# Optimization experiments

Hardware: AMD Instinct MI355X
Metric: run time of the kernel (lower is better)

The kernel has to match this reference:

```python
import jax, jax.numpy as jnp
import numpy as np

V, D, L, H, FF, B, S = 32000, 2048, 4, 16, 8192, 2, 2048
DH = D // H
PRUNE_LAYERS = (1, 2)   # layers with an attached pruning module
KEEP_RATIO = 0.5        # keep_ratio arg of forward_prefill_with_pruning


def _rms(x, w, eps=1e-6):
    return x * w * jax.lax.rsqrt(jnp.mean(x * x, -1, keepdims=True) + eps)


def _rope(x):
    # x: [B,H,s,DH]; position_ids = arange(s), recomputed after every pruning step
    s = x.shape[2]
    half = DH // 2
    inv = 1.0 / (10000.0 ** (jnp.arange(half, dtype=jnp.float32) / half))
    ang = jnp.arange(s, dtype=jnp.float32)[:, None] * inv  # [s, half]
    cos, sin = jnp.cos(ang), jnp.sin(ang)
    x1, x2 = x[..., :half], x[..., half:]
    return jnp.concatenate([x1 * cos - x2 * sin, x1 * sin + x2 * cos], -1)


def _block(h, mask, wq, wk, wv, wo, wg, wu, wd, ln1, ln2):
    b, s, _ = h.shape
    hn = _rms(h, ln1)
    q = _rope((hn @ wq).reshape(b, s, H, DH).transpose(0, 2, 1, 3))
    k = _rope((hn @ wk).reshape(b, s, H, DH).transpose(0, 2, 1, 3))
    v = (hn @ wv).reshape(b, s, H, DH).transpose(0, 2, 1, 3)
    att = jnp.einsum('bhqd,bhkd->bhqk', q, k) / np.float32(np.sqrt(DH))
    allowed = jnp.tril(jnp.ones((s, s), bool)) & (mask[:, None, None, :] > 0)
    att = jnp.where(allowed, att, jnp.float32(-1e9))
    o = jnp.einsum('bhqk,bhkd->bhqd', jax.nn.softmax(att, -1), v)
    h = h + o.transpose(0, 2, 1, 3).reshape(b, s, D) @ wo
    hn = _rms(h, ln2)
    h = h + (jax.nn.silu(hn @ wg) * (hn @ wu)) @ wd
    return h


def _forward(input_ids, attention_mask, embed, wq, wk, wv, wo, wg, wu, wd, ln1, ln2, lnf, lm_head, scorer):
    h = embed[input_ids]        # [B,S,D]
    mask = attention_mask
    for i in range(L):
        if i in PRUNE_LAYERS:
            pi = PRUNE_LAYERS.index(i)
            # pruning module: Linear(D->2); keep score = logits[..., 0]
            sc = jnp.einsum('bsd,cd->bsc', h, scorer[pi])[..., 0]
            kk = max(1, int(h.shape[1] * KEEP_RATIO))      # static under jit
            _, idx = jax.lax.top_k(sc, kk)
            idx = jnp.sort(idx, -1)                        # sorted kept indices
            h = jnp.take_along_axis(h, idx[..., None], axis=1)
            mask = jnp.take_along_axis(mask, idx, axis=1)
        h = _block(h, mask, wq[i], wk[i], wv[i], wo[i], wg[i], wu[i], wd[i], ln1[i], ln2[i])
    return _rms(h, lnf) @ lm_head   # logits [B, S_pruned, V]


def setup_inputs() -> dict:
    key = jax.random.key(0)
    ks = jax.random.split(key, 12)
    g = lambda k, shape: jax.random.normal(k, shape, jnp.float32) * 0.02
    return {
        'input_ids': jax.random.randint(ks[0], (B, S), 0, V, jnp.int32),
        'attention_mask': jnp.ones((B, S), jnp.int32),
        'embed': g(ks[1], (V, D)),
        'wq': g(ks[2], (L, D, D)),
        'wk': g(ks[3], (L, D, D)),
        'wv': g(ks[4], (L, D, D)),
        'wo': g(ks[5], (L, D, D)),
        'wg': g(ks[6], (L, D, FF)),
        'wu': g(ks[7], (L, D, FF)),
        'wd': g(ks[8], (L, FF, D)),
        'ln1': jnp.ones((L, D), jnp.float32),
        'ln2': jnp.ones((L, D), jnp.float32),
        'lnf': jnp.ones((D,), jnp.float32),
        'lm_head': g(ks[9], (D, V)),
        'scorer': g(ks[10], (len(PRUNE_LAYERS), 2, D)),
    }


def reference(input_ids, attention_mask, embed, wq, wk, wv, wo, wg, wu, wd, ln1, ln2, lnf, lm_head, scorer):
    return _forward(input_ids, attention_mask, embed, wq, wk, wv, wo, wg, wu, wd, ln1, ln2, lnf, lm_head, scorer)
```

## Files before the change

### kernel.cpp

```cpp
#include <hip/hip_runtime.h>
#include <math.h>


#define DD 2048
#define HH 16
#define DHH 128
#define FFF 8192
#define BBATCH 2
#define SSEQ 2048
#define VV 32000
#define LLAYERS 4

typedef float4 f4;
typedef __attribute__((ext_vector_type(8))) short short8;
typedef __attribute__((ext_vector_type(4))) float f32x4;
typedef unsigned short u16;

__device__ inline u16 bf16rne(float x) {
    unsigned u = __float_as_uint(x);
    unsigned r = (u + 0x7FFFu + ((u >> 16) & 1u)) >> 16;
    return (u16)r;
}
__device__ inline float bf16tof(u16 h) {
    return __uint_as_float(((unsigned)h) << 16);
}

__device__ __forceinline__ void gload16(const u16* g, u16* l) {
    __builtin_amdgcn_global_load_lds(
        (const __attribute__((address_space(1))) unsigned int*)g,
        (__attribute__((address_space(3))) unsigned int*)l, 16, 0, 0);
}

#define BARRIER() do { asm volatile("" ::: "memory"); \
    __builtin_amdgcn_s_barrier(); asm volatile("" ::: "memory"); } while (0)

__device__ __forceinline__ void xcd_swz(int& bx, int& by) {
    int gy = gridDim.y;
    int nwg = gridDim.x * gy;
    int orig = bx * gy + by;
    int q = nwg >> 3, r = nwg & 7;
    int xcd = orig & 7, loc = orig >> 3;
    int swz = (xcd < r ? xcd * (q + 1) : r * (q + 1) + (xcd - r) * q) + loc;
    bx = swz / gy;
    by = swz % gy;
}

__global__ void k_embed(const int* __restrict__ ids, const float* __restrict__ emb,
                        float* __restrict__ out) {
    int row = blockIdx.x;
    int id  = ids[row];
    const f4* src = (const f4*)(emb + (size_t)id * DD);
    f4*       dst = (f4*)(out + (size_t)row * DD);
    for (int i = threadIdx.x; i < DD / 4; i += blockDim.x) dst[i] = src[i];
}

__global__ void k_copy_int(const int* __restrict__ src, int* __restrict__ dst, int n) {
    int i = blockIdx.x * blockDim.x + threadIdx.x;
    if (i < n) dst[i] = src[i];
}

__global__ void k_addN(float* __restrict__ H, const float* __restrict__ P,
                       long len, int nparts) {
    long i = (long)blockIdx.x * 256 + threadIdx.x;
    if (i >= len / 4) return;
    f4 h = ((f4*)H)[i];
    for (int z = 0; z < nparts; z++) {
        f4 p = ((const f4*)(P + (size_t)z * len))[i];
        h.x += p.x; h.y += p.y; h.z += p.z; h.w += p.w;
    }
    ((f4*)H)[i] = h;
}

__global__ __launch_bounds__(256) void k_rmsnorm_cvt(const float* __restrict__ x,
                                                     const float* __restrict__ w,
                                                     u16* __restrict__ OH,
                                                     u16* __restrict__ OL) {
    int row = blockIdx.x;
    const float* xr = x + (size_t)row * DD;
    float ss = 0.f;
    for (int i = threadIdx.x; i < DD / 4; i += blockDim.x) {
        f4 v = ((const f4*)xr)[i];
        ss += v.x * v.x + v.y * v.y + v.z * v.z + v.w * v.w;
    }
    for (int o = 32; o > 0; o >>= 1) ss += __shfl_down(ss, o);
    __shared__ float red[4];
    int wid = threadIdx.x >> 6, lane = threadIdx.x & 63;
    if (lane == 0) red[wid] = ss;
    __syncthreads();
    float tot = red[0] + red[1] + red[2] + red[3];
    float inv = 1.0f / sqrtf(tot / (float)DD + 1e-6f);
    for (int i = threadIdx.x; i < DD / 4; i += blockDim.x) {
        f4 v = ((const f4*)xr)[i];
        f4 wv = ((const f4*)w)[i];
        float o[4];
        o[0] = v.x * wv.x * inv; o[1] = v.y * wv.y * inv;
        o[2] = v.z * wv.z * inv; o[3] = v.w * wv.w * inv;
        ushort4 hv, lv;
        u16* hp = (u16*)&hv; u16* lp = (u16*)&lv;
#pragma unroll
        for (int j = 0; j < 4; j++) {
            u16 h = bf16rne(o[j]);
            hp[j] = h;
            lp[j] = bf16rne(o[j] - bf16tof(h));
        }
        *(ushort4*)&OH[(size_t)row * DD + i * 4] = hv;
        *(ushort4*)&OL[(size_t)row * DD + i * 4] = lv;
    }
}

__global__ __launch_bounds__(256) void k_cvt_w(const float* __restrict__ W,
                                               u16* __restrict__ WtH,
                                               u16* __restrict__ WtL,
                                               int K, int N, int nc0, int dn0,
                                               int writeLo) {
    __shared__ float T[64][65];
    int tid = threadIdx.x;
    int n0g = nc0 + blockIdx.x * 64;
    int k0  = blockIdx.y * 64;
#pragma unroll
    for (int it = 0; it < 4; it++) {
        int r = it * 16 + (tid >> 4);
        int c4 = (tid & 15) * 4;
        f4 v = *(const f4*)(W + (size_t)(k0 + r) * N + n0g + c4);
        T[r][c4 + 0] = v.x; T[r][c4 + 1] = v.y;
        T[r][c4 + 2] = v.z; T[r][c4 + 3] = v.w;
    }
    __syncthreads();
    int nl = tid >> 2;
    int ks = (tid & 3) * 16;
    u16 hi[16], lo[16];
#pragma unroll
    for (int j = 0; j < 16; j++) {
        float v = T[ks + j][nl];
        u16 h = bf16rne(v);
        hi[j] = h;
        lo[j] = bf16rne(v - bf16tof(h));
    }
    size_t base = (size_t)(dn0 + blockIdx.x * 64 + nl) * K + k0 + ks;
    *(short8*)&WtH[base]     = *(short8*)&hi[0];
    *(short8*)&WtH[base + 8] = *(short8*)&hi[8];
    if (writeLo) {
        *(short8*)&WtL[base]     = *(short8*)&lo[0];
        *(short8*)&WtL[base + 8] = *(short8*)&lo[8];
    }
}

template <int PASSES, int RES, int DUAL>
__global__ __launch_bounds__(256, 2) void k_bgemm(const u16* __restrict__ AH,
                                                  const u16* __restrict__ AL,
                                                  const u16* __restrict__ B1H,
                                                  const u16* __restrict__ B1L,
                                                  const u16* __restrict__ B2H,
                                                  const u16* __restrict__ B2L,
                                                  const float* __restrict__ Rsrc,
                                                  float* __restrict__ C,
                                                  u16* __restrict__ OH,
                                                  u16* __restrict__ OL,
                                                  int M, int ldC, int K) {
    constexpr int NW = DUAL ? 2 : 1;
    __shared__ u16 As[128 * 32];
    __shared__ u16 Bs[NW][128 * 32];
    int tid = threadIdx.x;
    int bx = blockIdx.x, by = blockIdx.y;
    xcd_swz(bx, by);
    int m0 = by * 128, n0 = bx * 128;
    int lane = tid & 63, w = tid >> 6;
    int wm = w >> 1, wn = w & 1;
    int lr = lane & 15, lq = lane >> 4;
    int grow = lane >> 2;
    int gcol = (lane & 3) * 8;

    f32x4 acc[NW][4][4];
#pragma unroll
    for (int u = 0; u < NW; u++)
#pragma unroll
        for (int i = 0; i < 4; i++)
#pragma unroll
            for (int j = 0; j < 4; j++)
#pragma unroll
                for (int r = 0; r < 4; r++) acc[u][i][j][r] = 0.f;

    const int KT = PASSES * K;
    for (int kb = 0; kb < KT; kb += 32) {
        int p  = (PASSES > 1) ? ((kb >= 2 * K) ? 2 : ((kb >= K) ? 1 : 0)) : 0;
        int ks = kb - p * K;
        const u16* Ab = ((p == 2) ? AL  : AH)  + (size_t)(m0 + w * 32) * K + ks;
        const u16* Bb = ((p == 1) ? B1L : B1H) + (size_t)(n0 + w * 32) * K + ks;
        __syncthreads();
        gload16(Ab + (size_t)grow * K + gcol,        &As[w * 1024]);
        gload16(Ab + (size_t)(grow + 16) * K + gcol, &As[w * 1024 + 512]);
        gload16(Bb + (size_t)grow * K + gcol,        &Bs[0][w * 1024]);
        gload16(Bb + (size_t)(grow + 16) * K + gcol, &Bs[0][w * 1024 + 512]);
        if constexpr (DUAL) {
            const u16* B2b = ((p == 1) ? B2L : B2H) + (size_t)(n0 + w * 32) * K + ks;
            gload16(B2b + (size_t)grow * K + gcol,        &Bs[1][w * 1024]);
            gload16(B2b + (size_t)(grow + 16) * K + gcol, &Bs[1][w * 1024 + 512]);
        }
        __syncthreads();
        short8 a[4];
#pragma unroll
        for (int i = 0; i < 4; i++)
            a[i] = *(const short8*)&As[(wm * 64 + i * 16 + lr) * 32 + lq * 8];
#pragma unroll
        for (int u = 0; u < NW; u++) {
#pragma unroll
            for (int j = 0; j < 4; j++) {
                short8 b = *(const short8*)&Bs[u][(wn * 64 + j * 16 + lr) * 32 + lq * 8];
#pragma unroll
                for (int i = 0; i < 4; i++)
                    acc[u][i][j] = __builtin_amdgcn_mfma_f32_16x16x32_bf16(
                        a[i], b, acc[u][i][j], 0, 0, 0);
            }
        }
    }
#pragma unroll
    for (int i = 0; i < 4; i++) {
#pragma unroll
        for (int j = 0; j < 4; j++) {
            int gm = m0 + wm * 64 + i * 16 + lq * 4;
            int gn = n0 + wn * 64 + j * 16 + lr;
#pragma unroll
            for (int r = 0; r < 4; r++) {
                size_t off = (size_t)(gm + r) * ldC + gn;
                if constexpr (DUAL) {
                    float g = acc[0][i][j][r], uu = acc[1][i][j][r];
                    float v = g / (1.0f + expf(-g)) * uu;
                    u16 h = bf16rne(v);
                    OH[off] = h;
                    OL[off] = bf16rne(v - bf16tof(h));
                } else {
                    float v = acc[0][i][j][r];
                    if constexpr (RES) v += Rsrc[off];
                    C[off] = v;
                }
            }
        }
    }
}

template <int PASSES, int PLANE, int EPI>
__global__ __launch_bounds__(512, 2) void k_bg256(const u16* __restrict__ AH,
                                                  const u16* __restrict__ AL,
                                                  const u16* __restrict__ BH,
                                                  const u16* __restrict__ BL,
                                                  float* __restrict__ C,
                                                  u16* __restrict__ OH,
                                                  u16* __restrict__ OL,
                                                  const u16* __restrict__ GEH,
                                                  const u16* __restrict__ GEL,
                                                  int M, int ldC, int K, int ld) {
    __shared__ u16 SM[65536];
    int tid = threadIdx.x;
    int bx = blockIdx.x, by = blockIdx.y;
    xcd_swz(bx, by);
    {
        size_t zo = (size_t)blockIdx.z * K;
        AH += zo; BH += zo;
        if constexpr (PASSES > 1) { AL += zo; BL += zo; }
        if constexpr (!PLANE) C += (size_t)blockIdx.z * ((size_t)M * ldC);
    }
    int m0 = by * 256, n0 = bx * 256;
    int w = tid >> 6, lane = tid & 63;
    int wm = w >> 2, wn = w & 3;
    int lr = lane & 15, lq = lane >> 4;

    f32x4 acc[8][4];
#pragma unroll
    for (int i = 0; i < 8; i++)
#pragma unroll
        for (int j = 0; j < 4; j++)
#pragma unroll
            for (int r = 0; r < 4; r++) acc[i][j][r] = 0.f;

    auto ASRC = [&](int T) -> const u16* {
        int kb = T * 64;
        if (PASSES > 1) {
            if (kb >= 2 * K) return AL + (kb - 2 * K);
            if (kb >= K)     return AH + (kb - K);
        }
        return AH + kb;
    };
    auto BSRC = [&](int T) -> const u16* {
        int kb = T * 64;
        if (PASSES > 1) {
            if (kb >= 2 * K) return BH + (kb - 2 * K);
            if (kb >= K)     return BL + (kb - K);
        }
        return BH + kb;
    };
    int srr = lane >> 3;
    int scc = ((lane & 7) ^ srr) * 8;
    auto STAGE_A = [&](int T, int h, int buf) {
        const u16* s = ASRC(T) + (size_t)(m0 + h * 128 + w * 16 + srr) * ld + scc;
        u16* d = SM + buf * 32768 + h * 8192 + w * 16 * 64;
        gload16(s, d);
        gload16(s + (size_t)8 * ld, d + 8 * 64);
    };
    auto STAGE_B = [&](int T, int h, int buf) {
        const u16* s = BSRC(T) + (size_t)(n0 + h * 128 + w * 16 + srr) * ld + scc;
        u16* d = SM + buf * 32768 + 16384 + h * 8192 + w * 16 * 64;
        gload16(s, d);
        gload16(s + (size_t)8 * ld, d + 8 * 64);
    };
    auto RD_A = [&](const u16* SMb, int MH, short8 (&aF)[4][2]) {
        const u16* Ab = SMb + MH * 8192;
#pragma unroll
        for (int i = 0; i < 4; i++)
#pragma unroll
            for (int kk = 0; kk < 2; kk++)
                aF[i][kk] = *(const short8*)&Ab[(wm * 64 + i * 16 + lr) * 64 +
                                                (((kk * 4 + lq) ^ (lr & 7)) * 8)];
    };
    auto RD_B = [&](const u16* SMb, int NH, short8 (&bF)[2][2]) {
        const u16* Bb = SMb + 16384 + NH * 8192;
#pragma unroll
        for (int j = 0; j < 2; j++)
#pragma unroll
            for (int kk = 0; kk < 2; kk++)
                bF[j][kk] = *(const short8*)&Bb[(wn * 32 + j * 16 + lr) * 64 +
                                                (((kk * 4 + lq) ^ (lr & 7)) * 8)];
    };

    const int NT = (PASSES * K) >> 6;
    STAGE_A(0, 0, 0); STAGE_B(0, 0, 0);
    STAGE_A(0, 1, 0); STAGE_B(0, 1, 0);
    asm volatile("s_waitcnt vmcnt(0)" ::: "memory");
    BARRIER();

    for (int T = 0; T < NT; T++) {
        int cur = T & 1;
        const u16* SMb = SM + cur * 32768;
        short8 a0[4][2], a1[4][2], b0[2][2], b1[2][2];
        if (T + 1 < NT) { STAGE_A(T + 1, 0, cur ^ 1); STAGE_B(T + 1, 0, cur ^ 1); }
        RD_A(SMb, 0, a0);
        RD_B(SMb, 0, b0);
        if (T + 1 < NT) { STAGE_A(T + 1, 1, cur ^ 1); STAGE_B(T + 1, 1, cur ^ 1); }
        RD_B(SMb, 1, b1);
        RD_A(SMb, 1, a1);
        __builtin_amdgcn_s_setprio(1);
#pragma unroll
        for (int kk = 0; kk < 2; kk++)
#pragma unroll
            for (int j = 0; j < 2; j++)
#pragma unroll
                for (int i = 0; i < 4; i++)
                    acc[i][j] = __builtin_amdgcn_mfma_f32_16x16x32_bf16(
                        a0[i][kk], b0[j][kk], acc[i][j], 0, 0, 0);
#pragma unroll
        for (int kk = 0; kk < 2; kk++)
#pragma unroll
            for (int j = 0; j < 2; j++)
#pragma unroll
                for (int i = 0; i < 4; i++)
                    acc[i][2 + j] = __builtin_amdgcn_mfma_f32_16x16x32_bf16(
                        a0[i][kk], b1[j][kk], acc[i][2 + j], 0, 0, 0);
#pragma unroll
        for (int kk = 0; kk < 2; kk++)
#pragma unroll
            for (int j = 0; j < 2; j++)
#pragma unroll
                for (int i = 0; i < 4; i++)
                    acc[4 + i][j] = __builtin_amdgcn_mfma_f32_16x16x32_bf16(
                        a1[i][kk], b0[j][kk], acc[4 + i][j], 0, 0, 0);
#pragma unroll
        for (int kk = 0; kk < 2; kk++)
#pragma unroll
            for (int j = 0; j < 2; j++)
#pragma unroll
                for (int i = 0; i < 4; i++)
                    acc[4 + i][2 + j] = __builtin_amdgcn_mfma_f32_16x16x32_bf16(
                        a1[i][kk], b1[j][kk], acc[4 + i][2 + j], 0, 0, 0);
        __builtin_amdgcn_s_setprio(0);
        if (T + 1 < NT) {
            asm volatile("s_waitcnt vmcnt(0)" ::: "memory");
            BARRIER();
        }
    }

#pragma unroll
    for (int i16 = 0; i16 < 8; i16++) {
#pragma unroll
        for (int jj = 0; jj < 4; jj++) {
            int gm = m0 + (i16 >> 2) * 128 + wm * 64 + (i16 & 3) * 16 + lq * 4;
            int gn = n0 + (jj >> 1) * 128 + wn * 32 + (jj & 1) * 16 + lr;
#pragma unroll
            for (int r = 0; r < 4; r++) {
                size_t off = (size_t)(gm + r) * ldC + gn;
                float v = acc[i16][jj][r];
                if constexpr (PLANE) {
                    if constexpr (EPI) {
                        float g = bf16tof(GEH[off]) + bf16tof(GEL[off]);
                        v = g / (1.0f + expf(-g)) * v;
                    }
                    u16 h = bf16rne(v);
                    OH[off] = h;
                    OL[off] = bf16rne(v - bf16tof(h));
                } else {
                    C[off] = v;
                }
            }
        }
    }
}

__global__ void k_rope_table(float* __restrict__ cosT, float* __restrict__ sinT) {
    int idx = blockIdx.x * blockDim.x + threadIdx.x;
    if (idx >= SSEQ * 64) return;
    int pos = idx >> 6, d = idx & 63;
    float p   = (float)pow(10000.0, (double)d * (1.0 / 64.0));
    float inv = 1.0f / p;
    float ang = (float)pos * inv;
    cosT[idx] = (float)cos((double)ang);
    sinT[idx] = (float)sin((double)ang);
}

__global__ void k_rope(float* __restrict__ C,
                       const float* __restrict__ cosT, const float* __restrict__ sinT,
                       int s, int ld) {
    int bi = blockIdx.x;
    int h = bi % HH;
    int i = (bi / HH) % s;
    size_t base = (size_t)(bi / HH) * ld + h * DHH;
    int d = threadIdx.x;
    float c  = cosT[i * 64 + d];
    float sn = sinT[i * 64 + d];
    float x1 = C[base + d], x2 = C[base + 64 + d];
    C[base + d]      = x1 * c - x2 * sn;
    C[base + 64 + d] = x1 * sn + x2 * c;
    x1 = C[base + 2048 + d]; x2 = C[base + 2048 + 64 + d];
    C[base + 2048 + d]      = x1 * c - x2 * sn;
    C[base + 2048 + 64 + d] = x1 * sn + x2 * c;
}

__global__ __launch_bounds__(256) void k_cvt_qkr(const float* __restrict__ C,
                                                 const float* __restrict__ cosT,
                                                 const float* __restrict__ sinT,
                                                 u16* __restrict__ QHp, u16* __restrict__ QLp,
                                                 u16* __restrict__ KHp, u16* __restrict__ KLp,
                                                 int s) {
    int row = blockIdx.x;
    int i = row % s;
    int c = threadIdx.x * 8;
    int d = c & 127;
    int hi2 = (d >= 64) ? 1 : 0;
    int dd = d - hi2 * 64;
    const float* tb = cosT + (size_t)i * 64;
    const float* ts = sinT + (size_t)i * 64;
#pragma unroll
    for (int sec = 0; sec < 2; sec++) {
        const float* src = C + (size_t)row * 6144 + sec * 2048;
        int base1 = c - hi2 * 64;
        float o[8];
#pragma unroll
        for (int q = 0; q < 2; q++) {
            f4 v1 = *(const f4*)(src + base1 + q * 4);
            f4 v2 = *(const f4*)(src + base1 + 64 + q * 4);
            float a1[4] = {v1.x, v1.y, v1.z, v1.w};
            float a2[4] = {v2.x, v2.y, v2.z, v2.w};
#pragma unroll
            for (int e = 0; e < 4; e++) {
                float cc = tb[dd + q * 4 + e];
                float sn = ts[dd + q * 4 + e];
                o[q * 4 + e] = hi2 ? (a1[e] * sn + a2[e] * cc)
                                   : (a1[e] * cc - a2[e] * sn);
            }
        }
        u16 hbuf[8], lbuf[8];
#pragma unroll
        for (int e = 0; e < 8; e++) {
            u16 h = bf16rne(o[e]);
            hbuf[e] = h;
            lbuf[e] = bf16rne(o[e] - bf16tof(h));
        }
        u16* dh = (sec ? KHp : QHp) + (size_t)row * 2048 + c;
        u16* dl = (sec ? KLp : QLp) + (size_t)row * 2048 + c;
        *(short8*)dh = *(short8*)&hbuf[0];
        *(short8*)dl = *(short8*)&lbuf[0];
    }
}

__global__ __launch_bounds__(256) void k_cvt_vt(const float* __restrict__ C,
                                                u16* __restrict__ VtH,
                                                u16* __restrict__ VtL, int s) {
    __shared__ float T[64][132];
    int bh = blockIdx.y;
    int h = bh & 15, b = bh >> 4;
    int kv0 = blockIdx.x * 64;
    int t = threadIdx.x;
#pragma unroll
    for (int it = 0; it < 8; it++) {
        int kv = it * 8 + (t >> 5);
        int c4 = (t & 31) * 4;
        f4 v = *(const f4*)(C + (size_t)((size_t)b * s + kv0 + kv) * 6144 + 4096 + h * 128 + c4);
        T[kv][c4 + 0] = v.x; T[kv][c4 + 1] = v.y;
        T[kv][c4 + 2] = v.z; T[kv][c4 + 3] = v.w;
    }
    __syncthreads();
    int d = t >> 1, seg = t & 1;
    size_t base = ((size_t)bh * 128 + d) * s + kv0 + seg * 32;
#pragma unroll
    for (int g = 0; g < 4; g++) {
        u16 h8[8], l8[8];
#pragma unroll
        for (int e = 0; e < 8; e++) {
            float v = T[seg * 32 + g * 8 + e][d];
            u16 hh = bf16rne(v);
            h8[e] = hh;
            l8[e] = bf16rne(v - bf16tof(hh));
        }
        int gp = (g ^ ((d >> 1) & 3)) * 8;
        *(short8*)&VtH[base + gp] = *(short8*)&h8[0];
        *(short8*)&VtL[base + gp] = *(short8*)&l8[0];
    }
}

template <int PASSES>
__global__ __launch_bounds__(256, 2) void k_attn_mfma(
        const u16* __restrict__ QHp, const u16* __restrict__ QLp,
        const u16* __restrict__ KHp, const u16* __restrict__ KLp,
        const u16* __restrict__ VtH, const u16* __restrict__ VtL,
        const int* __restrict__ mask,
        u16* __restrict__ OH, u16* __restrict__ OL, int s) {
    constexpr int BUFU = (PASSES > 1) ? 16384 : 8192;
    constexpr int VOFF = (PASSES > 1) ? 8192 : 4096;
    __shared__ u16 SM[2 * BUFU + 5120];
    int tid = threadIdx.x, lane = tid & 63, w = tid >> 6;
    int lr = lane & 15, lq = lane >> 4;
    int grow = lane >> 2;
    int sgcol = (((lane & 3) ^ ((lane >> 3) & 3))) * 8;
    int gcol  = (lane & 3) * 8;
    int rc = (lq ^ ((lr >> 1) & 3)) * 8;
    int gx = gridDim.x;
    int NB = gx * gridDim.y;
    int orig = blockIdx.y * gx + blockIdx.x;
    int qq = NB >> 3, rr = NB & 7;
    int xcd = orig & 7, loc = orig >> 3;
    int swz = (xcd < rr ? xcd * (qq + 1) : rr * (qq + 1) + (xcd - rr) * qq) + loc;
    int bh = swz / gx;
    int qt = gx - 1 - (swz % gx);
    int h = bh & 15, b = bh >> 4;
    int q0 = qt * 128;
    size_t rb = (size_t)b * s;
    const u16* vtH = VtH + (size_t)bh * 128 * s;
    const u16* vtL = VtL + (size_t)bh * 128 * s;
    u16* PHw = SM + 2 * BUFU + w * 1280;
    u16* PLw = PHw + 640;
    const float scale = 0.08838834764831845f;

    short8 qh[2][4], ql[2][4];
#pragma unroll
    for (int st = 0; st < 2; st++) {
        const u16* qp = QHp + (rb + q0 + st * 64) * 2048 + h * 128 + w * 32;
#pragma unroll
        for (int it = 0; it < 4; it++)
            gload16(qp + (size_t)(it * 16 + grow) * 2048 + sgcol, SM + w * 2048 + it * 512);
        __syncthreads();
#pragma unroll
        for (int ks = 0; ks < 4; ks++)
            qh[st][ks] = *(const short8*)&SM[ks * 2048 + (w * 16 + lr) * 32 + rc];
        if constexpr (PASSES > 1) {
            __syncthreads();
            const u16* qp2 = QLp + (rb + q0 + st * 64) * 2048 + h * 128 + w * 32;
#pragma unroll
            for (int it = 0; it < 4; it++)
                gload16(qp2 + (size_t)(it * 16 + grow) * 2048 + sgcol, SM + w * 2048 + it * 512);
            __syncthreads();
#pragma unroll
            for (int ks = 0; ks < 4; ks++)
                ql[st][ks] = *(const short8*)&SM[ks * 2048 + (w * 16 + lr) * 32 + rc];
        }
        __syncthreads();
    }

    auto kv_stage = [&](int t, int buf) {
        u16* base = SM + buf * BUFU;
        const u16* kp = KHp + (rb + t * 32) * 2048 + h * 128 + w * 32;
        gload16(kp + (size_t)grow * 2048 + sgcol,        base + w * 1024);
        gload16(kp + (size_t)(16 + grow) * 2048 + sgcol, base + w * 1024 + 512);
        const u16* vp = vtH + (size_t)(w * 32) * s + t * 32;
        gload16(vp + (size_t)grow * s + gcol,        base + VOFF + (w * 32) * 32);
        gload16(vp + (size_t)(16 + grow) * s + gcol, base + VOFF + (w * 32 + 16) * 32);
        if constexpr (PASSES > 1) {
            const u16* kp2 = KLp + (rb + t * 32) * 2048 + h * 128 + w * 32;
            gload16(kp2 + (size_t)grow * 2048 + sgcol,        base + 4096 + w * 1024);
            gload16(kp2 + (size_t)(16 + grow) * 2048 + sgcol, base + 4096 + w * 1024 + 512);
            const u16* vp2 = vtL + (size_t)(w * 32) * s + t * 32;
            gload16(vp2 + (size_t)grow * s + gcol,        base + 12288 + (w * 32) * 32);
            gload16(vp2 + (size_t)(16 + grow) * s + gcol, base + 12288 + (w * 32 + 16) * 32);
        }
    };

    f32x4 o_acc[2][8];
#pragma unroll
    for (int st = 0; st < 2; st++)
#pragma unroll
        for (int j = 0; j < 8; j++)
#pragma unroll
            for (int r = 0; r < 4; r++) o_acc[st][j][r] = 0.f;
    float m_run[2][4], l_run[2][4];
#pragma unroll
    for (int st = 0; st < 2; st++)
#pragma unroll
        for (int r = 0; r < 4; r++) { m_run[st][r] = -3.0e38f; l_run[st][r] = 0.f; }

    int nt = (q0 + 128) >> 5;
    int mv0 = mask[rb + lr];
    int mv1 = mask[rb + 16 + lr];
    kv_stage(0, 0);
    for (int t = 0; t < nt; t++) {
        int bsel = t & 1;
        if (t + 1 < nt) {
            kv_stage(t + 1, 1 - bsel);
            if constexpr (PASSES > 1)
                asm volatile("s_waitcnt vmcnt(8)" ::: "memory");
            else
                asm volatile("s_waitcnt vmcnt(4)" ::: "memory");
        } else {
            asm volatile("s_waitcnt vmcnt(0)" ::: "memory");
        }
        BARRIER();
        int nmv0 = mv0, nmv1 = mv1;
        if (t + 1 < nt) {
            nmv0 = mask[rb + (t + 1) * 32 + lr];
            nmv1 = mask[rb + (t + 1) * 32 + 16 + lr];
        }
        const u16* KsH = SM + bsel * BUFU;
        const u16* KsL = KsH + 4096;
        const u16* VsH = SM + bsel * BUFU + VOFF;
        const u16* VsL = SM + bsel * BUFU + 12288;
#pragma unroll
        for (int st = 0; st < 2; st++) {
            if (t * 32 > q0 + st * 64 + w * 16 + 15) continue;
            f32x4 sa[2];
#pragma unroll
            for (int j = 0; j < 2; j++)
#pragma unroll
                for (int r = 0; r < 4; r++) sa[j][r] = 0.f;
#pragma unroll
            for (int j = 0; j < 2; j++) {
#pragma unroll
                for (int ks = 0; ks < 4; ks++) {
                    short8 kb = *(const short8*)&KsH[ks * 1024 + (j * 16 + lr) * 32 + rc];
                    sa[j] = __builtin_amdgcn_mfma_f32_16x16x32_bf16(qh[st][ks], kb, sa[j], 0, 0, 0);
                    if constexpr (PASSES > 1) {
                        short8 kl2 = *(const short8*)&KsL[ks * 1024 + (j * 16 + lr) * 32 + rc];
                        sa[j] = __builtin_amdgcn_mfma_f32_16x16x32_bf16(qh[st][ks], kl2, sa[j], 0, 0, 0);
                        sa[j] = __builtin_amdgcn_mfma_f32_16x16x32_bf16(ql[st][ks], kb, sa[j], 0, 0, 0);
                    }
                }
            }
            float sclv[4];
#pragma unroll
            for (int r = 0; r < 4; r++) {
                int ig = q0 + st * 64 + w * 16 + lq * 4 + r;
                float v0 = (t * 32 + lr <= ig && mv0 > 0) ? sa[0][r] * scale : -1.0e9f;
                float v1 = (t * 32 + 16 + lr <= ig && mv1 > 0) ? sa[1][r] * scale : -1.0e9f;
                float mx = fmaxf(v0, v1);
                mx = fmaxf(mx, __shfl_xor(mx, 1));
                mx = fmaxf(mx, __shfl_xor(mx, 2));
                mx = fmaxf(mx, __shfl_xor(mx, 4));
                mx = fmaxf(mx, __shfl_xor(mx, 8));
                float mo = m_run[st][r];
                float mn = fmaxf(mo, mx);
                float p0 = expf(v0 - mn), p1 = expf(v1 - mn);
                float ps = p0 + p1;
                ps += __shfl_xor(ps, 1);
                ps += __shfl_xor(ps, 2);
                ps += __shfl_xor(ps, 4);
                ps += __shfl_xor(ps, 8);
                sclv[r] = expf(mo - mn);
                m_run[st][r] = mn;
                l_run[st][r] = l_run[st][r] * sclv[r] + ps;
                int prow = lq * 4 + r;
                u16 h0 = bf16rne(p0);
                u16 h1 = bf16rne(p1);
                PHw[prow * 40 + lr] = h0;
                PHw[prow * 40 + 16 + lr] = h1;
                if constexpr (PASSES > 1) {
                    PLw[prow * 40 + lr] = bf16rne(p0 - bf16tof(h0));
                    PLw[prow * 40 + 16 + lr] = bf16rne(p1 - bf16tof(h1));
                }
            }
#pragma unroll
            for (int j = 0; j < 8; j++)
#pragma unroll
                for (int r = 0; r < 4; r++) o_acc[st][j][r] *= sclv[r];
            short8 ph = *(const short8*)&PHw[lr * 40 + lq * 8];
            short8 pl;
            if constexpr (PASSES > 1) pl = *(const short8*)&PLw[lr * 40 + lq * 8];
#pragma unroll
            for (int j = 0; j < 8; j++) {
                int vrow = j * 16 + lr;
                short8 vh = *(const short8*)&VsH[vrow * 32 + rc];
                o_acc[st][j] = __builtin_amdgcn_mfma_f32_16x16x32_bf16(ph, vh, o_acc[st][j], 0, 0, 0);
                if constexpr (PASSES > 1) {
                    short8 vl = *(const short8*)&VsL[vrow * 32 + rc];
                    o_acc[st][j] = __builtin_amdgcn_mfma_f32_16x16x32_bf16(ph, vl, o_acc[st][j], 0, 0, 0);
                    o_acc[st][j] = __builtin_amdgcn_mfma_f32_16x16x32_bf16(pl, vh, o_acc[st][j], 0, 0, 0);
                }
            }
        }
        BARRIER();
        mv0 = nmv0; mv1 = nmv1;
    }
#pragma unroll
    for (int st = 0; st < 2; st++) {
#pragma unroll
        for (int r = 0; r < 4; r++) {
            float linv = 1.0f / l_run[st][r];
            size_t rowoff = (rb + q0 + st * 64 + w * 16 + lq * 4 + r) * 2048 + h * 128 + lr;
#pragma unroll
            for (int j = 0; j < 8; j++) {
                float v = o_acc[st][j][r] * linv;
                u16 hh = bf16rne(v);
                OH[rowoff + j * 16] = hh;
                OL[rowoff + j * 16] = bf16rne(v - bf16tof(hh));
            }
        }
    }
}

__global__ __launch_bounds__(256, 2) void k_attn_f32(const float* __restrict__ Q,
                                                     const float* __restrict__ K,
                                                     const float* __restrict__ V,
                                                     const int* __restrict__ mask,
                                                     u16* __restrict__ OH,
                                                     u16* __restrict__ OL, int s, int ld) {
    int qt = blockIdx.x, bh = blockIdx.y;
    int h = bh & (HH - 1), b = bh >> 4;
    __shared__ float Qs[64][132];
    __shared__ float Ks[32 * 128];
    __shared__ float Vs[32][132];
    __shared__ float Ps[64][36];
    __shared__ float mrow[64], lrow[64];
    int tid = threadIdx.x;
    int tx = tid & 15, ty = tid >> 4;

#pragma unroll
    for (int p = 0; p < 2; p++) {
        int r = p * 32 + (tid >> 3);
        int kb = (tid & 7) * 4;
        const float* src = Q + (size_t)(b * s + qt * 64 + r) * ld + h * DHH;
#pragma unroll
        for (int q = 0; q < 4; q++)
            *(f4*)&Qs[r][kb + 32 * q] = *(const f4*)(src + kb + 32 * q);
    }
    if (tid < 64) { mrow[tid] = -3.0e38f; lrow[tid] = 0.f; }

    float acc[4][8];
#pragma unroll
    for (int i = 0; i < 4; i++)
#pragma unroll
        for (int c = 0; c < 8; c++) acc[i][c] = 0.f;
    const float scale = 0.08838834764831845f;

    int ktmax = 2 * (qt + 1);
    for (int kt = 0; kt < ktmax; kt++) {
        __syncthreads();
#pragma unroll
        for (int p = 0; p < 4; p++) {
            int c = p * 8 + (tid >> 5);
            int kk = (tid & 31) * 4;
            size_t g = (size_t)(b * s + kt * 32 + c) * ld + h * DHH + kk;
            f4 kv = *(const f4*)(K + g);
            int ch = (kk >> 2) ^ (c >> 1);
            *(f4*)&Ks[c * 128 + ch * 4] = kv;
            *(f4*)&Vs[c][kk] = *(const f4*)(V + g);
        }
        __syncthreads();
        float sv[4][2];
#pragma unroll
        for (int i = 0; i < 4; i++) { sv[i][0] = 0.f; sv[i][1] = 0.f; }
        for (int kk = 0; kk < 128; kk += 4) {
            f4 qv[4];
#pragma unroll
            for (int i = 0; i < 4; i++) qv[i] = *(const f4*)&Qs[ty * 4 + i][kk];
#pragma unroll
            for (int j = 0; j < 2; j++) {
                int c = tx * 2 + j;
                int ch = (kk >> 2) ^ (c >> 1);
                f4 kv = *(const f4*)&Ks[c * 128 + ch * 4];
#pragma unroll
                for (int i = 0; i < 4; i++)
                    sv[i][j] += qv[i].x * kv.x + qv[i].y * kv.y +
                                qv[i].z * kv.z + qv[i].w * kv.w;
            }
        }
        float scl[4];
#pragma unroll
        for (int i = 0; i < 4; i++) {
            int r = ty * 4 + i;
            int igl = qt * 64 + r;
#pragma unroll
            for (int j = 0; j < 2; j++) {
                int jg = kt * 32 + tx * 2 + j;
                bool ok = (jg <= igl) && (mask[b * s + jg] > 0);
                sv[i][j] = ok ? sv[i][j] * scale : -1.0e9f;
            }
            float rmax = fmaxf(sv[i][0], sv[i][1]);
            rmax = fmaxf(rmax, __shfl_xor(rmax, 1));
            rmax = fmaxf(rmax, __shfl_xor(rmax, 2));
            rmax = fmaxf(rmax, __shfl_xor(rmax, 4));
            rmax = fmaxf(rmax, __shfl_xor(rmax, 8));
            float mold = mrow[r];
            float mnew = fmaxf(mold, rmax);
            float p0 = expf(sv[i][0] - mnew);
            float p1 = expf(sv[i][1] - mnew);
            float ps = p0 + p1;
            ps += __shfl_xor(ps, 1);
            ps += __shfl_xor(ps, 2);
            ps += __shfl_xor(ps, 4);
            ps += __shfl_xor(ps, 8);
            scl[i] = expf(mold - mnew);
            if (tx == 0) { mrow[r] = mnew; lrow[r] = lrow[r] * scl[i] + ps; }
            float2 pw; pw.x = p0; pw.y = p1;
            *(float2*)&Ps[r][tx * 2] = pw;
        }
        __syncthreads();
#pragma unroll
        for (int i = 0; i < 4; i++) {
            float sc = scl[i];
#pragma unroll
            for (int c = 0; c < 8; c++) acc[i][c] *= sc;
        }
        for (int jj = 0; jj < 32; jj += 4) {
            f4 pv[4];
#pragma unroll
            for (int i = 0; i < 4; i++) pv[i] = *(const f4*)&Ps[ty * 4 + i][jj];
#pragma unroll
            for (int j2 = 0; j2 < 4; j2++) {
                f4 va = *(const f4*)&Vs[jj + j2][tx * 4];
                f4 vb = *(const f4*)&Vs[jj + j2][64 + tx * 4];
#pragma unroll
                for (int i = 0; i < 4; i++) {
                    float p = (&pv[i].x)[j2];
                    acc[i][0] += p * va.x; acc[i][1] += p * va.y;
                    acc[i][2] += p * va.z; acc[i][3] += p * va.w;
                    acc[i][4] += p * vb.x; acc[i][5] += p * vb.y;
                    acc[i][6] += p * vb.z; acc[i][7] += p * vb.w;
                }
            }
        }
    }
    __syncthreads();
#pragma unroll
    for (int i = 0; i < 4; i++) {
        int r = ty * 4 + i;
        float linv = 1.0f / lrow[r];
        size_t ob = (size_t)(b * s + qt * 64 + r) * DD + h * DHH;
        ushort4 h1, l1, h2, l2;
        u16 *h1p = (u16*)&h1, *l1p = (u16*)&l1, *h2p = (u16*)&h2, *l2p = (u16*)&l2;
#pragma unroll
        for (int c = 0; c < 4; c++) {
            float v = acc[i][c] * linv;
            u16 hh = bf16rne(v);
            h1p[c] = hh; l1p[c] = bf16rne(v - bf16tof(hh));
            float v2 = acc[i][c + 4] * linv;
            u16 hh2 = bf16rne(v2);
            h2p[c] = hh2; l2p[c] = bf16rne(v2 - bf16tof(hh2));
        }
        *(ushort4*)&OH[ob + tx * 4] = h1;
        *(ushort4*)&OL[ob + tx * 4] = l1;
        *(ushort4*)&OH[ob + 64 + tx * 4] = h2;
        *(ushort4*)&OL[ob + 64 + tx * 4] = l2;
    }
}

__global__ __launch_bounds__(256) void k_score(const float* __restrict__ Hb,
                                               const float* __restrict__ srow,
                                               float* __restrict__ sc) {
    int row = blockIdx.x;
    const float* xr = Hb + (size_t)row * DD;
    float ss = 0.f;
    for (int i = threadIdx.x; i < DD / 4; i += blockDim.x) {
        f4 a = ((const f4*)xr)[i];
        f4 w = ((const f4*)srow)[i];
        ss += a.x * w.x + a.y * w.y + a.z * w.z + a.w * w.w;
    }
    for (int o = 32; o > 0; o >>= 1) ss += __shfl_down(ss, o);
    __shared__ float red[4];
    int wid = threadIdx.x >> 6, lane = threadIdx.x & 63;
    if (lane == 0) red[wid] = ss;
    __syncthreads();
    if (threadIdx.x == 0) sc[row] = red[0] + red[1] + red[2] + red[3];
}

__global__ __launch_bounds__(256) void k_rank(const float* __restrict__ sc,
                                              int* __restrict__ flg, int s, int kk) {
    int b = blockIdx.x / s, i = blockIdx.x % s;
    const float* scb = sc + (size_t)b * s;
    float vi = scb[i];
    int cnt = 0;
    for (int j = threadIdx.x; j < s; j += 256) {
        float vj = scb[j];
        if (vj > vi || (vj == vi && j < i)) cnt++;
    }
    for (int o = 32; o > 0; o >>= 1) cnt += __shfl_down(cnt, o);
    __shared__ int red[4];
    int wid = threadIdx.x >> 6, lane = threadIdx.x & 63;
    if (lane == 0) red[wid] = cnt;
    __syncthreads();
    if (threadIdx.x == 0) flg[b * s + i] = ((red[0] + red[1] + red[2] + red[3]) < kk) ? 1 : 0;
}

__global__ void k_compact(const int* __restrict__ flg, int* __restrict__ idx, int s, int kk) {
    int b = blockIdx.x;
    if (threadIdx.x == 0) {
        int p = 0;
        for (int i = 0; i < s; i++)
            if (flg[b * s + i]) idx[b * kk + (p++)] = i;
    }
}

__global__ void k_gather(const float* __restrict__ Hin, const int* __restrict__ idx,
                         float* __restrict__ Hout, int s, int kk) {
    int row = blockIdx.x;
    int b = row / kk, p = row % kk;
    int i = idx[b * kk + p];
    const f4* src = (const f4*)(Hin + (size_t)(b * s + i) * DD);
    f4* dst = (f4*)(Hout + (size_t)row * DD);
    for (int t = threadIdx.x; t < DD / 4; t += blockDim.x) dst[t] = src[t];
}

__global__ void k_gather_mask(const int* __restrict__ Min, const int* __restrict__ idx,
                              int* __restrict__ Mout, int s, int kk) {
    int t = blockIdx.x * blockDim.x + threadIdx.x;
    if (t < BBATCH * kk) {
        int b = t / kk, p = t % kk;
        Mout[t] = Min[b * s + idx[b * kk + p]];
    }
}

extern "C" void kernel_launch(void* const* d_in, const int* in_sizes, int n_in,
                              void* d_out, int out_size, void* d_ws, size_t ws_size,
                              hipStream_t stream) {
    const int*   input_ids = (const int*)d_in[0];
    const int*   attn_mask = (const int*)d_in[1];
    const float* embed     = (const float*)d_in[2];
    const float* wq        = (const float*)d_in[3];
    const float* wk        = (const float*)d_in[4];
    const float* wv        = (const float*)d_in[5];
    const float* wo        = (const float*)d_in[6];
    const float* wg        = (const float*)d_in[7];
    const float* wu        = (const float*)d_in[8];
    const float* wd        = (const float*)d_in[9];
    const float* ln1       = (const float*)d_in[10];
    const float* ln2       = (const float*)d_in[11];
    const float* lnf       = (const float*)d_in[12];
    const float* lm_head   = (const float*)d_in[13];
    const float* scorer    = (const float*)d_in[14];

    float* ws = (float*)d_ws;
    const size_t R = (size_t)BBATCH * SSEQ * DD;
    const size_t MISC_FLOATS = 2 * SSEQ * 64 + 5 * (size_t)BBATCH * SSEQ + 1024;
    const size_t NEED_A = (14 * R + MISC_FLOATS) * 4;
    const bool bigws = (ws_size >= NEED_A);

    float* H0   = ws;
    float* H1   = ws + R;
    float* CQKV = ws + 2 * R;
    u16*   AH   = (u16*)(ws + 5 * R);
    u16*   AL   = AH + (size_t)4096 * DD;

    u16* QHp = (u16*)(ws + 6 * R);
    u16* QLp = QHp + (size_t)4096 * DD;
    u16* KHp = (u16*)(ws + 7 * R);
    u16* KLp = KHp + (size_t)4096 * DD;
    u16* VtH = (u16*)(ws + 8 * R);
    u16* VtL = VtH + (size_t)4096 * DD;
    u16* FH  = (u16*)(ws + 6 * R);
    u16* FL  = (u16*)(ws + 8 * R);
    u16* WH1 = (u16*)(ws + 10 * R);
    u16* WL1 = WH1 + (size_t)FFF * DD;
    u16* WH2 = (u16*)(ws + 12 * R);
    u16* WL2 = WH2 + (size_t)FFF * DD;
    u16* WDH = (u16*)(ws + 10 * R);
    u16* WDL = WDH + (size_t)DD * FFF;
    u16* WQKVH = (u16*)(ws + 10 * R);
    u16* WQKVL = WQKVH + (size_t)6144 * DD;

    u16* cWgH = (u16*)CQKV;
    u16* cWgL = cWgH + (size_t)2048 * DD;
    u16* cWuH = cWgL + (size_t)2048 * DD;
    u16* cWuL = cWuH + (size_t)2048 * DD;
    u16* cFH  = (u16*)(ws + 3 * R);
    u16* cFL  = cFH + (size_t)4096 * 2048;
    u16* cWdH = (u16*)(ws + 4 * R);
    u16* cWdL = cWdH + (size_t)2048 * DD;

    float* miscB = ws + (bigws ? 14 * R : 6 * R);
    float* COS = miscB;
    float* SIN = COS + SSEQ * 64;
    float* SC  = SIN + SSEQ * 64;
    int*   FLG = (int*)(SC + (size_t)BBATCH * SSEQ);
    int*   IDX = FLG + BBATCH * SSEQ;
    int*   M0  = IDX + BBATCH * SSEQ;
    int*   M1  = M0 + BBATCH * SSEQ;

    k_rope_table<<<(SSEQ * 64 + 255) / 256, 256, 0, stream>>>(COS, SIN);
    k_embed<<<BBATCH * SSEQ, 256, 0, stream>>>(input_ids, embed, H0);
    k_copy_int<<<(BBATCH * SSEQ + 255) / 256, 256, 0, stream>>>(attn_mask, M0, BBATCH * SSEQ);

    float* Hc = H0; float* Nc = H1;
    int*   Mc = M0; int*   Mt = M1;
    int s = SSEQ;

    for (int l = 0; l < LLAYERS; l++) {
        if (l == 1 || l == 2) {
            int pi = l - 1;
            int kk = s / 2;
            k_score<<<BBATCH * s, 256, 0, stream>>>(Hc, scorer + (size_t)pi * 2 * DD, SC);
            k_rank<<<BBATCH * s, 256, 0, stream>>>(SC, FLG, s, kk);
            k_compact<<<BBATCH, 64, 0, stream>>>(FLG, IDX, s, kk);
            k_gather<<<BBATCH * kk, 256, 0, stream>>>(Hc, IDX, Nc, s, kk);
            k_gather_mask<<<(BBATCH * kk + 255) / 256, 256, 0, stream>>>(Mc, IDX, Mt, s, kk);
            { float* t = Hc; Hc = Nc; Nc = t; }
            { int* t = Mc; Mc = Mt; Mt = t; }
            s = kk;
        }
        int rows = BBATCH * s;
        const bool hiP = (l < 2);
        const int wlo = hiP ? 1 : 0;
        const float* Wq = wq + (size_t)l * DD * DD;
        const float* Wk = wk + (size_t)l * DD * DD;
        const float* Wv = wv + (size_t)l * DD * DD;
        const float* Wo = wo + (size_t)l * DD * DD;
        const float* Wg = wg + (size_t)l * DD * FFF;
        const float* Wu = wu + (size_t)l * DD * FFF;
        const float* Wd = wd + (size_t)l * FFF * DD;
        const float* L1 = ln1 + (size_t)l * DD;
        const float* L2 = ln2 + (size_t)l * DD;

        dim3 gWd(DD / 64, DD / 64);

        k_rmsnorm_cvt<<<rows, 256, 0, stream>>>(Hc, L1, AH, AL);
        if (bigws) {
            k_cvt_w<<<gWd, 256, 0, stream>>>(Wq, WQKVH, WQKVL, DD, DD, 0, 0, wlo);
            k_cvt_w<<<gWd, 256, 0, stream>>>(Wk, WQKVH, WQKVL, DD, DD, 0, 2048, wlo);
            k_cvt_w<<<gWd, 256, 0, stream>>>(Wv, WQKVH, WQKVL, DD, DD, 0, 4096, wlo);
            if (rows >= 2048) {
                dim3 gQKV(6144 / 256, rows / 256);
                if (hiP) k_bg256<3,0,0><<<gQKV,512,0,stream>>>(AH,AL,WQKVH,WQKVL,CQKV,nullptr,nullptr,nullptr,nullptr,rows,6144,DD,DD);
                else     k_bg256<1,0,0><<<gQKV,512,0,stream>>>(AH,AL,WQKVH,WQKVL,CQKV,nullptr,nullptr,nullptr,nullptr,rows,6144,DD,DD);
            } else {
                dim3 gQKV(6144 / 128, rows / 128);
                k_bgemm<1,0,0><<<gQKV,256,0,stream>>>(AH,AL,WQKVH,WQKVL,nullptr,nullptr,nullptr,CQKV,nullptr,nullptr,rows,6144,DD);
            }
        } else {
            u16* WtH = (u16*)Nc;
            u16* WtL = WtH + (size_t)DD * DD;
            dim3 gG(DD / 128, rows / 128);
            const float* Wqkv[3] = {Wq, Wk, Wv};
            for (int q3 = 0; q3 < 3; q3++) {
                k_cvt_w<<<gWd, 256, 0, stream>>>(Wqkv[q3], WtH, WtL, DD, DD, 0, 0, wlo);
                float* Cb = CQKV + q3 * 2048;
                if (hiP) k_bgemm<3,0,0><<<gG,256,0,stream>>>(AH,AL,WtH,WtL,nullptr,nullptr,nullptr,Cb,nullptr,nullptr,rows,6144,DD);
                else     k_bgemm<1,0,0><<<gG,256,0,stream>>>(AH,AL,WtH,WtL,nullptr,nullptr,nullptr,Cb,nullptr,nullptr,rows,6144,DD);
            }
        }

        if (bigws) {
            k_cvt_qkr<<<rows, 256, 0, stream>>>(CQKV, COS, SIN, QHp, QLp, KHp, KLp, s);
            k_cvt_vt<<<dim3(s / 64, BBATCH * HH), 256, 0, stream>>>(CQKV, VtH, VtL, s);
            if (hiP) k_attn_mfma<3><<<dim3(s / 128, BBATCH * HH), 256, 0, stream>>>(
                         QHp, QLp, KHp, KLp, VtH, VtL, Mc, AH, AL, s);
            else     k_attn_mfma<1><<<dim3(s / 128, BBATCH * HH), 256, 0, stream>>>(
                         QHp, QLp, KHp, KLp, VtH, VtL, Mc, AH, AL, s);
        } else {
            k_rope<<<rows * HH, 64, 0, stream>>>(CQKV, COS, SIN, s, 6144);
            k_attn_f32<<<dim3(s / 64, BBATCH * HH), 256, 0, stream>>>(
                CQKV, CQKV + 2048, CQKV + 4096, Mc, AH, AL, s, 6144);
        }

        {
            u16* WtH = bigws ? WQKVH : (u16*)Nc;
            u16* WtL = bigws ? (WQKVH + (size_t)DD * DD) : ((u16*)Nc + (size_t)DD * DD);
            k_cvt_w<<<gWd, 256, 0, stream>>>(Wo, WtH, WtL, DD, DD, 0, 0, wlo);
            if (bigws && hiP) {
                int SK = (rows >= 4096) ? 2 : 4;
                float* P = ws + 2 * R;
                dim3 g(DD / 256, rows / 256, SK);
                k_bg256<3,0,0><<<g, 512, 0, stream>>>(AH, AL, WtH, WtL, P,
                                                      nullptr, nullptr, nullptr, nullptr,
                                                      rows, DD, DD / SK, DD);
                long len = (long)rows * DD;
                k_addN<<<(len / 4 + 255) / 256, 256, 0, stream>>>(Hc, P, len, SK);
            } else {
                dim3 gG(DD / 128, rows / 128);
                if (hiP) k_bgemm<3,1,0><<<gG,256,0,stream>>>(AH,AL,WtH,WtL,nullptr,nullptr,Hc,Hc,nullptr,nullptr,rows,DD,DD);
                else     k_bgemm<1,1,0><<<gG,256,0,stream>>>(AH,AL,WtH,WtL,nullptr,nullptr,Hc,Hc,nullptr,nullptr,rows,DD,DD);
            }
        }

        k_rmsnorm_cvt<<<rows, 256, 0, stream>>>(Hc, L2, AH, AL);
        if (bigws && rows >= 2048) {
            k_cvt_w<<<dim3(FFF / 64, DD / 64), 256, 0, stream>>>(Wg, WH1, WL1, DD, FFF, 0, 0, wlo);
            k_cvt_w<<<dim3(FFF / 64, DD / 64), 256, 0, stream>>>(Wu, WH2, WL2, DD, FFF, 0, 0, wlo);
            u16* Gh = (l == 0) ? (u16*)(ws + R) : (u16*)(ws + 2 * R);
            u16* Gl = (u16*)(ws + 3 * R);
            dim3 gMLP(FFF / 256, rows / 256);
            if (hiP) {
                k_bg256<3,1,0><<<gMLP,512,0,stream>>>(AH,AL,WH1,WL1,nullptr,Gh,Gl,nullptr,nullptr,rows,FFF,DD,DD);
                k_bg256<3,1,1><<<gMLP,512,0,stream>>>(AH,AL,WH2,WL2,nullptr,FH,FL,Gh,Gl,rows,FFF,DD,DD);
            } else {
                k_bg256<1,1,0><<<gMLP,512,0,stream>>>(AH,AL,WH1,WL1,nullptr,Gh,Gl,nullptr,nullptr,rows,FFF,DD,DD);
                k_bg256<1,1,1><<<gMLP,512,0,stream>>>(AH,AL,WH2,WL2,nullptr,FH,FL,Gh,Gl,rows,FFF,DD,DD);
            }
            k_cvt_w<<<dim3(DD / 64, FFF / 64), 256, 0, stream>>>(Wd, WDH, WDL, FFF, DD, 0, 0, wlo);
            int SK = (rows >= 4096) ? 2 : 4;
            float* P = ws + 2 * R;
            dim3 gD(DD / 256, rows / 256, SK);
            if (hiP) k_bg256<3,0,0><<<gD,512,0,stream>>>(FH,FL,WDH,WDL,P,nullptr,nullptr,nullptr,nullptr,rows,DD,FFF/SK,FFF);
            else     k_bg256<1,0,0><<<gD,512,0,stream>>>(FH,FL,WDH,WDL,P,nullptr,nullptr,nullptr,nullptr,rows,DD,FFF/SK,FFF);
            long len = (long)rows * DD;
            k_addN<<<(len / 4 + 255) / 256, 256, 0, stream>>>(Hc, P, len, SK);
        } else if (bigws) {
            k_cvt_w<<<dim3(FFF / 64, DD / 64), 256, 0, stream>>>(Wg, WH1, WL1, DD, FFF, 0, 0, wlo);
            k_cvt_w<<<dim3(FFF / 64, DD / 64), 256, 0, stream>>>(Wu, WH2, WL2, DD, FFF, 0, 0, wlo);
            k_bgemm<1,0,1><<<dim3(FFF/128, rows/128),256,0,stream>>>(AH,AL,WH1,WL1,WH2,WL2,nullptr,nullptr,FH,FL,rows,FFF,DD);
            k_cvt_w<<<dim3(DD / 64, FFF / 64), 256, 0, stream>>>(Wd, WDH, WDL, FFF, DD, 0, 0, wlo);
            k_bgemm<1,1,0><<<dim3(DD/128, rows/128),256,0,stream>>>(FH,FL,WDH,WDL,nullptr,nullptr,Hc,Hc,nullptr,nullptr,rows,DD,FFF);
        } else {
            for (int ffc = 0; ffc < FFF; ffc += 2048) {
                k_cvt_w<<<dim3(2048 / 64, DD / 64), 256, 0, stream>>>(Wg, cWgH, cWgL, DD, FFF, ffc, 0, wlo);
                k_cvt_w<<<dim3(2048 / 64, DD / 64), 256, 0, stream>>>(Wu, cWuH, cWuL, DD, FFF, ffc, 0, wlo);
                if (hiP) k_bgemm<3,0,1><<<dim3(16, rows/128),256,0,stream>>>(AH,AL,cWgH,cWgL,cWuH,cWuL,nullptr,nullptr,cFH,cFL,rows,2048,DD);
                else     k_bgemm<1,0,1><<<dim3(16, rows/128),256,0,stream>>>(AH,AL,cWgH,cWgL,cWuH,cWuL,nullptr,nullptr,cFH,cFL,rows,2048,DD);
                k_cvt_w<<<dim3(DD / 64, 2048 / 64), 256, 0, stream>>>(Wd + (size_t)ffc * DD, cWdH, cWdL, 2048, DD, 0, 0, wlo);
                if (hiP) k_bgemm<3,1,0><<<dim3(DD/128, rows/128),256,0,stream>>>(cFH,cFL,cWdH,cWdL,nullptr,nullptr,Hc,Hc,nullptr,nullptr,rows,DD,2048);
                else     k_bgemm<1,1,0><<<dim3(DD/128, rows/128),256,0,stream>>>(cFH,cFL,cWdH,cWdL,nullptr,nullptr,Hc,Hc,nullptr,nullptr,rows,DD,2048);
            }
        }
    }

    int rows = BBATCH * s;
    u16* AHf = (u16*)Nc;
    u16* ALf = AHf + (size_t)rows * DD;
    u16* LmH = bigws ? (u16*)(ws + 6 * R) : (u16*)CQKV;
    k_rmsnorm_cvt<<<rows, 256, 0, stream>>>(Hc, lnf, AHf, ALf);
    k_cvt_w<<<dim3(VV / 64, DD / 64), 256, 0, stream>>>(lm_head, LmH, LmH, DD, VV, 0, 0, 0);
    if (bigws) {
        k_bg256<1,0,0><<<dim3(VV / 256, rows / 256), 512, 0, stream>>>(
            AHf, ALf, LmH, LmH, (float*)d_out, nullptr, nullptr, nullptr, nullptr,
            rows, VV, DD, DD);
    } else {
        k_bgemm<1,0,0><<<dim3(VV / 128, rows / 128), 256, 0, stream>>>(
            AHf, ALf, LmH, LmH, nullptr, nullptr, nullptr, (float*)d_out,
            nullptr, nullptr, rows, VV, DD);
    }
}
```

Measured before the change: 4.528 ms.

## Switch GEMM main loop to 4-stage LDS ring with BK=32 tiles

```diff
diff --git a/kernel.cpp b/kernel.cpp
--- a/kernel.cpp
+++ b/kernel.cpp
@@ -263,6 +263,7 @@
     int w = tid >> 6, lane = tid & 63;
     int wm = w >> 2, wn = w & 3;
     int lr = lane & 15, lq = lane >> 4;
+    int rc = (lq ^ ((lr >> 1) & 3)) * 8;
 
     f32x4 acc[8][4];
 #pragma unroll
@@ -273,7 +274,7 @@
             for (int r = 0; r < 4; r++) acc[i][j][r] = 0.f;
 
     auto ASRC = [&](int T) -> const u16* {
-        int kb = T * 64;
+        int kb = T * 32;
         if (PASSES > 1) {
             if (kb >= 2 * K) return AL + (kb - 2 * K);
             if (kb >= K)     return AH + (kb - K);
@@ -281,98 +282,58 @@
         return AH + kb;
     };
     auto BSRC = [&](int T) -> const u16* {
-        int kb = T * 64;
+        int kb = T * 32;
         if (PASSES > 1) {
             if (kb >= 2 * K) return BH + (kb - 2 * K);
             if (kb >= K)     return BL + (kb - K);
         }
         return BH + kb;
     };
-    int srr = lane >> 3;
-    int scc = ((lane & 7) ^ srr) * 8;
-    auto STAGE_A = [&](int T, int h, int buf) {
-        const u16* s = ASRC(T) + (size_t)(m0 + h * 128 + w * 16 + srr) * ld + scc;
-        u16* d = SM + buf * 32768 + h * 8192 + w * 16 * 64;
-        gload16(s, d);
-        gload16(s + (size_t)8 * ld, d + 8 * 64);
+    int srr = lane >> 2;
+    int scc = (((lane & 3) ^ ((lane >> 3) & 3))) * 8;
+    auto STAGE = [&](int T, int buf) {
+        const u16* sa = ASRC(T) + (size_t)(m0 + w * 32 + srr) * ld + scc;
+        u16* da = SM + buf * 16384 + (w * 32) * 32;
+        gload16(sa, da);
+        gload16(sa + (size_t)16 * ld, da + 16 * 32);
+        const u16* sb = BSRC(T) + (size_t)(n0 + w * 32 + srr) * ld + scc;
+        u16* db = SM + buf * 16384 + 8192 + (w * 32) * 32;
+        gload16(sb, db);
+        gload16(sb + (size_t)16 * ld, db + 16 * 32);
     };
-    auto STAGE_B = [&](int T, int h, int buf) {
-        const u16* s = BSRC(T) + (size_t)(n0 + h * 128 + w * 16 + srr) * ld + scc;
-        u16* d = SM + buf * 32768 + 16384 + h * 8192 + w * 16 * 64;
-        gload16(s, d);
-        gload16(s + (size_t)8 * ld, d + 8 * 64);
-    };
-    auto RD_A = [&](const u16* SMb, int MH, short8 (&aF)[4][2]) {
-        const u16* Ab = SMb + MH * 8192;
-#pragma unroll
-        for (int i = 0; i < 4; i++)
-#pragma unroll
-            for (int kk = 0; kk < 2; kk++)
-                aF[i][kk] = *(const short8*)&Ab[(wm * 64 + i * 16 + lr) * 64 +
-                                                (((kk * 4 + lq) ^ (lr & 7)) * 8)];
-    };
-    auto RD_B = [&](const u16* SMb, int NH, short8 (&bF)[2][2]) {
-        const u16* Bb = SMb + 16384 + NH * 8192;
-#pragma unroll
-        for (int j = 0; j < 2; j++)
-#pragma unroll
-            for (int kk = 0; kk < 2; kk++)
-                bF[j][kk] = *(const short8*)&Bb[(wn * 32 + j * 16 + lr) * 64 +
-                                                (((kk * 4 + lq) ^ (lr & 7)) * 8)];
-    };
-
-    const int NT = (PASSES * K) >> 6;
-    STAGE_A(0, 0, 0); STAGE_B(0, 0, 0);
-    STAGE_A(0, 1, 0); STAGE_B(0, 1, 0);
-    asm volatile("s_waitcnt vmcnt(0)" ::: "memory");
+
+    const int NT = (PASSES * K) >> 5;
+    STAGE(0, 0); STAGE(1, 1); STAGE(2, 2);
+    asm volatile("s_waitcnt vmcnt(8)" ::: "memory");
     BARRIER();
 
     for (int T = 0; T < NT; T++) {
-        int cur = T & 1;
-        const u16* SMb = SM + cur * 32768;
-        short8 a0[4][2], a1[4][2], b0[2][2], b1[2][2];
-        if (T + 1 < NT) { STAGE_A(T + 1, 0, cur ^ 1); STAGE_B(T + 1, 0, cur ^ 1); }
-        RD_A(SMb, 0, a0);
-        RD_B(SMb, 0, b0);
-        if (T + 1 < NT) { STAGE_A(T + 1, 1, cur ^ 1); STAGE_B(T + 1, 1, cur ^ 1); }
-        RD_B(SMb, 1, b1);
-        RD_A(SMb, 1, a1);
+        const u16* Ab = SM + (T & 3) * 16384;
+        const u16* Bb = Ab + 8192;
+        short8 aF[8], bF[4];
+#pragma unroll
+        for (int i = 0; i < 8; i++) {
+            int row = (i >> 2) * 128 + wm * 64 + (i & 3) * 16 + lr;
+            aF[i] = *(const short8*)&Ab[row * 32 + rc];
+        }
+        if (T + 3 < NT) STAGE(T + 3, (T + 3) & 3);
+#pragma unroll
+        for (int j = 0; j < 4; j++) {
+            int row = (j >> 1) * 128 + wn * 32 + (j & 1) * 16 + lr;
+            bF[j] = *(const short8*)&Bb[row * 32 + rc];
+        }
         __builtin_amdgcn_s_setprio(1);
 #pragma unroll
-        for (int kk = 0; kk < 2; kk++)
-#pragma unroll
-            for (int j = 0; j < 2; j++)
-#pragma unroll
-                for (int i = 0; i < 4; i++)
-                    acc[i][j] = __builtin_amdgcn_mfma_f32_16x16x32_bf16(
-                        a0[i][kk], b0[j][kk], acc[i][j], 0, 0, 0);
-#pragma unroll
-        for (int kk = 0; kk < 2; kk++)
-#pragma unroll
-            for (int j = 0; j < 2; j++)
-#pragma unroll
-                for (int i = 0; i < 4; i++)
-                    acc[i][2 + j] = __builtin_amdgcn_mfma_f32_16x16x32_bf16(
-                        a0[i][kk], b1[j][kk], acc[i][2 + j], 0, 0, 0);
-#pragma unroll
-        for (int kk = 0; kk < 2; kk++)
-#pragma unroll
-            for (int j = 0; j < 2; j++)
-#pragma unroll
-                for (int i = 0; i < 4; i++)
-                    acc[4 + i][j] = __builtin_amdgcn_mfma_f32_16x16x32_bf16(
-                        a1[i][kk], b0[j][kk], acc[4 + i][j], 0, 0, 0);
-#pragma unroll
-        for (int kk = 0; kk < 2; kk++)
-#pragma unroll
-            for (int j = 0; j < 2; j++)
-#pragma unroll
-                for (int i = 0; i < 4; i++)
-                    acc[4 + i][2 + j] = __builtin_amdgcn_mfma_f32_16x16x32_bf16(
-                        a1[i][kk], b1[j][kk], acc[4 + i][2 + j], 0, 0, 0);
+        for (int j = 0; j < 4; j++)
+#pragma unroll
+            for (int i = 0; i < 8; i++)
+                acc[i][j] = __builtin_amdgcn_mfma_f32_16x16x32_bf16(
+                    aF[i], bF[j], acc[i][j], 0, 0, 0);
         __builtin_amdgcn_s_setprio(0);
         if (T + 1 < NT) {
-            asm volatile("s_waitcnt vmcnt(0)" ::: "memory");
+            if (T + 3 < NT)      asm volatile("s_waitcnt vmcnt(8)" ::: "memory");
+            else if (T + 2 < NT) asm volatile("s_waitcnt vmcnt(4)" ::: "memory");
+            else                 asm volatile("s_waitcnt vmcnt(0)" ::: "memory");
             BARRIER();
         }
     }
```

Result: slower. 4.723 ms (+4.3%).
